# Kernel optimization log

Hardware: AMD Instinct MI355X
Metric: run time of the kernel (lower is better)

Reference implementation:

```python
import jax, jax.numpy as jnp
import numpy as np

B, N, F = 256, 131072, 8


def setup_inputs() -> dict:
    key = jax.random.key(0)
    k1, k2 = jax.random.split(key)
    x = jax.random.normal(k1, (B, N), dtype=jnp.float32)
    # keras 'random_normal' initializer uses stddev=0.05; also keeps the IIR stable
    w = jax.random.normal(k2, (F,), dtype=jnp.float32) * 0.05
    return {"x": x, "w": w}


def reference(x, w):
    # Causal IIR recurrence:
    #   v[i] = 0                                   for i < F
    #   v[i] = x[i] + sum_{j=0}^{F-1} w[j] * v[i-j-1]   for i >= F
    # carry[:, j] holds v[i-1-j] for each batch row.
    Bx, Nx = x.shape
    Fw = w.shape[0]

    def step(carry, inp):
        xt, active = inp                      # xt: [B], active: scalar bool
        v = jnp.where(active, xt + carry @ w, jnp.zeros_like(xt))  # [B]
        new_carry = jnp.concatenate([v[:, None], carry[:, :-1]], axis=1)
        return new_carry, v

    carry0 = jnp.zeros((Bx, Fw), dtype=x.dtype)
    active = jnp.arange(Nx) >= Fw            # v[i]=0 until i >= filter_size
    _, ys = jax.lax.scan(step, carry0, (x.T, active))  # ys: [N, B]
    return ys.T                               # [B, N]
```

## Files before the change

kernel.cpp:

```cpp
#include <hip/hip_runtime.h>


constexpr int Bn   = 256;
constexpr int Nn   = 131072;
constexpr int Lc   = 16;
constexpr int Kn   = 32;
constexpr int TPB  = 256;
constexpr int SPAN = TPB * Lc;
constexpr int TROW = Nn / SPAN;
constexpr int PAD  = 20;

typedef float f32x4 __attribute__((ext_vector_type(4)));

#define IIR_STEP(vv, xx, a0,a1,a2,a3,a4,a5,a6,a7)                             \
    vv = fmaf(w0,(a0), fmaf(w1,(a1), fmaf(w2,(a2), fmaf(w3,(a3),              \
         fmaf(w4,(a4), fmaf(w5,(a5), fmaf(w6,(a6), fmaf(w7,(a7), (xx)))))))))

#define IIR_GROUP8(xa, xb)                                                    \
    IIR_STEP(v0, (xa).x, s0,s1,s2,s3,s4,s5,s6,s7);                            \
    IIR_STEP(v1, (xa).y, v0,s0,s1,s2,s3,s4,s5,s6);                            \
    IIR_STEP(v2, (xa).z, v1,v0,s0,s1,s2,s3,s4,s5);                            \
    IIR_STEP(v3, (xa).w, v2,v1,v0,s0,s1,s2,s3,s4);                            \
    IIR_STEP(v4, (xb).x, v3,v2,v1,v0,s0,s1,s2,s3);                            \
    IIR_STEP(v5, (xb).y, v4,v3,v2,v1,v0,s0,s1,s2);                            \
    IIR_STEP(v6, (xb).z, v5,v4,v3,v2,v1,v0,s0,s1);                            \
    IIR_STEP(v7, (xb).w, v6,v5,v4,v3,v2,v1,v0,s0);                            \
    s0=v7; s1=v6; s2=v5; s3=v4; s4=v3; s5=v2; s6=v1; s7=v0;

__global__ __launch_bounds__(256, 8)
void iir_kernel(const float* __restrict__ x,
                const float* __restrict__ wp,
                float* __restrict__ out) {
    __shared__ float tile[TPB * PAD];

    const int t = threadIdx.x;
    const int b = blockIdx.x;
    const size_t base = (size_t)b * SPAN;
    const bool row_start = ((b & (TROW - 1)) == 0);

    const float w0 = wp[0], w1 = wp[1], w2 = wp[2], w3 = wp[3],
                w4 = wp[4], w5 = wp[5], w6 = wp[6], w7 = wp[7];

    #pragma unroll
    for (int k = 0; k < 4; ++k) {
        const int f   = k * TPB + t;
        const float4 v = *reinterpret_cast<const float4*>(x + base + 4 * (size_t)f);
        const int c   = f >> 2;
        const int off = (f & 3) * 4;
        *reinterpret_cast<float4*>(&tile[c * PAD + off]) = v;
    }
    __syncthreads();

    float s0=0.f,s1=0.f,s2=0.f,s3=0.f,s4=0.f,s5=0.f,s6=0.f,s7=0.f;
    const int p = t * Lc;

    if (row_start && t == 0) {
    } else if (row_start && t < 3) {
        for (int e = 8; e < p; e += 8) {
            const float* lq = &tile[(e >> 4) * PAD + (e & 15)];
            float4 xa = *reinterpret_cast<const float4*>(lq);
            float4 xb = *reinterpret_cast<const float4*>(lq + 4);
            float v0,v1,v2,v3,v4,v5,v6,v7;
            IIR_GROUP8(xa, xb);
        }
    } else if (!row_start && t < 2) {
        const float* g = x + base + p - Kn;
        #pragma unroll
        for (int m = 0; m < Kn / 8; ++m) {
            float4 xa = *reinterpret_cast<const float4*>(g + 8 * m);
            float4 xb = *reinterpret_cast<const float4*>(g + 8 * m + 4);
            float v0,v1,v2,v3,v4,v5,v6,v7;
            IIR_GROUP8(xa, xb);
        }
    } else {
        #pragma unroll
        for (int cc = 0; cc < 2; ++cc) {
            const float* lq = &tile[(t - 2 + cc) * PAD];
            {
                float4 xa = *reinterpret_cast<const float4*>(lq);
                float4 xb = *reinterpret_cast<const float4*>(lq + 4);
                float v0,v1,v2,v3,v4,v5,v6,v7;
                IIR_GROUP8(xa, xb);
            }
            {
                float4 xa = *reinterpret_cast<const float4*>(lq + 8);
                float4 xb = *reinterpret_cast<const float4*>(lq + 12);
                float v0,v1,v2,v3,v4,v5,v6,v7;
                IIR_GROUP8(xa, xb);
            }
        }
    }
    __syncthreads();

    {
        float* lp = &tile[t * PAD];
        if (row_start && t == 0) {
            *reinterpret_cast<float4*>(lp)     = make_float4(0.f,0.f,0.f,0.f);
            *reinterpret_cast<float4*>(lp + 4) = make_float4(0.f,0.f,0.f,0.f);
        } else {
            float4 xa = *reinterpret_cast<const float4*>(lp);
            float4 xb = *reinterpret_cast<const float4*>(lp + 4);
            float v0,v1,v2,v3,v4,v5,v6,v7;
            IIR_GROUP8(xa, xb);
            *reinterpret_cast<float4*>(lp)     = make_float4(v0,v1,v2,v3);
            *reinterpret_cast<float4*>(lp + 4) = make_float4(v4,v5,v6,v7);
        }
        {
            float4 xa = *reinterpret_cast<const float4*>(lp + 8);
            float4 xb = *reinterpret_cast<const float4*>(lp + 12);
            float v0,v1,v2,v3,v4,v5,v6,v7;
            IIR_GROUP8(xa, xb);
            *reinterpret_cast<float4*>(lp + 8)  = make_float4(v0,v1,v2,v3);
            *reinterpret_cast<float4*>(lp + 12) = make_float4(v4,v5,v6,v7);
        }
    }
    __syncthreads();

    #pragma unroll
    for (int k = 0; k < 4; ++k) {
        const int f   = k * TPB + t;
        const int c   = f >> 2;
        const int off = (f & 3) * 4;
        const f32x4 v = *reinterpret_cast<const f32x4*>(&tile[c * PAD + off]);
        __builtin_nontemporal_store(v, reinterpret_cast<f32x4*>(out + base + 4 * (size_t)f));
    }
}

extern "C" void kernel_launch(void* const* d_in, const int* in_sizes, int n_in,
                              void* d_out, int out_size, void* d_ws, size_t ws_size,
                              hipStream_t stream) {
    const float* x = (const float*)d_in[0];
    const float* w = (const float*)d_in[1];
    float* out     = (float*)d_out;

    const int grid = (Bn * Nn) / SPAN;
    iir_kernel<<<grid, TPB, 0, stream>>>(x, w, out);
}
```

Measured before the change: 46.63 us.

## Load warmup and chunk inputs directly from global, drop staging barriers

Each thread now reads its 32-element warm-up window and its own 16-element chunk straight from global memory into registers, instead of first staging the whole block tile in shared memory behind two barriers. Only the computed outputs are written to shared memory for the coalesced nontemporal store. This removes the cooperative LDS load and two __syncthreads, at the cost of per-thread strided global reads that overlap neighbouring threads' data and rely on cache hits.

```diff
diff --git a/kernel.cpp b/kernel.cpp
--- a/kernel.cpp
+++ b/kernel.cpp
@@ -41,73 +41,69 @@
     const float w0 = wp[0], w1 = wp[1], w2 = wp[2], w3 = wp[3],
                 w4 = wp[4], w5 = wp[5], w6 = wp[6], w7 = wp[7];
 
-    #pragma unroll
-    for (int k = 0; k < 4; ++k) {
-        const int f   = k * TPB + t;
-        const float4 v = *reinterpret_cast<const float4*>(x + base + 4 * (size_t)f);
-        const int c   = f >> 2;
-        const int off = (f & 3) * 4;
-        *reinterpret_cast<float4*>(&tile[c * PAD + off]) = v;
-    }
-    __syncthreads();
-
     float s0=0.f,s1=0.f,s2=0.f,s3=0.f,s4=0.f,s5=0.f,s6=0.f,s7=0.f;
     const int p = t * Lc;
+    float* lp = &tile[t * PAD];
 
-    if (row_start && t == 0) {
-    } else if (row_start && t < 3) {
+    if (!row_start || t >= 3) {
+        const float* g = x + base + p - Kn;
+        const float4 a0 = *reinterpret_cast<const float4*>(g);
+        const float4 a1 = *reinterpret_cast<const float4*>(g + 4);
+        const float4 a2 = *reinterpret_cast<const float4*>(g + 8);
+        const float4 a3 = *reinterpret_cast<const float4*>(g + 12);
+        const float4 a4 = *reinterpret_cast<const float4*>(g + 16);
+        const float4 a5 = *reinterpret_cast<const float4*>(g + 20);
+        const float4 a6 = *reinterpret_cast<const float4*>(g + 24);
+        const float4 a7 = *reinterpret_cast<const float4*>(g + 28);
+        { float v0,v1,v2,v3,v4,v5,v6,v7; IIR_GROUP8(a0, a1); }
+        { float v0,v1,v2,v3,v4,v5,v6,v7; IIR_GROUP8(a2, a3); }
+        { float v0,v1,v2,v3,v4,v5,v6,v7; IIR_GROUP8(a4, a5); }
+        { float v0,v1,v2,v3,v4,v5,v6,v7; IIR_GROUP8(a6, a7); }
+        const float4 b0 = *reinterpret_cast<const float4*>(g + 32);
+        const float4 b1 = *reinterpret_cast<const float4*>(g + 36);
+        const float4 b2 = *reinterpret_cast<const float4*>(g + 40);
+        const float4 b3 = *reinterpret_cast<const float4*>(g + 44);
+        {
+            float v0,v1,v2,v3,v4,v5,v6,v7;
+            IIR_GROUP8(b0, b1);
+            *reinterpret_cast<float4*>(lp)     = make_float4(v0,v1,v2,v3);
+            *reinterpret_cast<float4*>(lp + 4) = make_float4(v4,v5,v6,v7);
+        }
+        {
+            float v0,v1,v2,v3,v4,v5,v6,v7;
+            IIR_GROUP8(b2, b3);
+            *reinterpret_cast<float4*>(lp + 8)  = make_float4(v0,v1,v2,v3);
+            *reinterpret_cast<float4*>(lp + 12) = make_float4(v4,v5,v6,v7);
+        }
+    } else if (t == 0) {
+        const float* g = x + base;
+        *reinterpret_cast<float4*>(lp)     = make_float4(0.f,0.f,0.f,0.f);
+        *reinterpret_cast<float4*>(lp + 4) = make_float4(0.f,0.f,0.f,0.f);
+        float4 xa = *reinterpret_cast<const float4*>(g + 8);
+        float4 xb = *reinterpret_cast<const float4*>(g + 12);
+        float v0,v1,v2,v3,v4,v5,v6,v7;
+        IIR_GROUP8(xa, xb);
+        *reinterpret_cast<float4*>(lp + 8)  = make_float4(v0,v1,v2,v3);
+        *reinterpret_cast<float4*>(lp + 12) = make_float4(v4,v5,v6,v7);
+    } else {
+        const float* g = x + base;
         for (int e = 8; e < p; e += 8) {
-            const float* lq = &tile[(e >> 4) * PAD + (e & 15)];
-            float4 xa = *reinterpret_cast<const float4*>(lq);
-            float4 xb = *reinterpret_cast<const float4*>(lq + 4);
+            float4 xa = *reinterpret_cast<const float4*>(g + e);
+            float4 xb = *reinterpret_cast<const float4*>(g + e + 4);
             float v0,v1,v2,v3,v4,v5,v6,v7;
             IIR_GROUP8(xa, xb);
         }
-    } else if (!row_start && t < 2) {
-        const float* g = x + base + p - Kn;
-        #pragma unroll
-        for (int m = 0; m < Kn / 8; ++m) {
-            float4 xa = *reinterpret_cast<const float4*>(g + 8 * m);
-            float4 xb = *reinterpret_cast<const float4*>(g + 8 * m + 4);
-            float v0,v1,v2,v3,v4,v5,v6,v7;
-            IIR_GROUP8(xa, xb);
-        }
-    } else {
-        #pragma unroll
-        for (int cc = 0; cc < 2; ++cc) {
-            const float* lq = &tile[(t - 2 + cc) * PAD];
-            {
-                float4 xa = *reinterpret_cast<const float4*>(lq);
-                float4 xb = *reinterpret_cast<const float4*>(lq + 4);
-                float v0,v1,v2,v3,v4,v5,v6,v7;
-                IIR_GROUP8(xa, xb);
-            }
-            {
-                float4 xa = *reinterpret_cast<const float4*>(lq + 8);
-                float4 xb = *reinterpret_cast<const float4*>(lq + 12);
-                float v0,v1,v2,v3,v4,v5,v6,v7;
-                IIR_GROUP8(xa, xb);
-            }
-        }
-    }
-    __syncthreads();
-
-    {
-        float* lp = &tile[t * PAD];
-        if (row_start && t == 0) {
-            *reinterpret_cast<float4*>(lp)     = make_float4(0.f,0.f,0.f,0.f);
-            *reinterpret_cast<float4*>(lp + 4) = make_float4(0.f,0.f,0.f,0.f);
-        } else {
-            float4 xa = *reinterpret_cast<const float4*>(lp);
-            float4 xb = *reinterpret_cast<const float4*>(lp + 4);
+        {
+            float4 xa = *reinterpret_cast<const float4*>(g + p);
+            float4 xb = *reinterpret_cast<const float4*>(g + p + 4);
             float v0,v1,v2,v3,v4,v5,v6,v7;
             IIR_GROUP8(xa, xb);
             *reinterpret_cast<float4*>(lp)     = make_float4(v0,v1,v2,v3);
             *reinterpret_cast<float4*>(lp + 4) = make_float4(v4,v5,v6,v7);
         }
         {
-            float4 xa = *reinterpret_cast<const float4*>(lp + 8);
-            float4 xb = *reinterpret_cast<const float4*>(lp + 12);
+            float4 xa = *reinterpret_cast<const float4*>(g + p + 8);
+            float4 xb = *reinterpret_cast<const float4*>(g + p + 12);
             float v0,v1,v2,v3,v4,v5,v6,v7;
             IIR_GROUP8(xa, xb);
             *reinterpret_cast<float4*>(lp + 8)  = make_float4(v0,v1,v2,v3);
```

Result: faster. 43.75 us (-6.2%).
